# Performance work log

Measured on AMD Instinct MI355X. Metric: run time of the kernel, lower is better.

## Reference

```python
import jax, jax.numpy as jnp
import numpy as np

H = 16  # num_heads

def setup_inputs() -> dict:
    key = jax.random.key(0)
    ks = jax.random.split(key, 9)
    B, S, E = 2, 2048, 1024
    d = E // H  # 64, shared KV head dim
    sc = lambda n: 1.0 / np.sqrt(n)
    return {
        "x": jax.random.normal(ks[0], (B, S, E), jnp.float32),
        "wq": jax.random.normal(ks[1], (E, E), jnp.float32) * sc(E),
        "bq": jax.random.normal(ks[2], (E,), jnp.float32) * 0.02,
        "wk": jax.random.normal(ks[3], (E, d), jnp.float32) * sc(E),
        "bk": jax.random.normal(ks[4], (d,), jnp.float32) * 0.02,
        "wv": jax.random.normal(ks[5], (E, d), jnp.float32) * sc(E),
        "bv": jax.random.normal(ks[6], (d,), jnp.float32) * 0.02,
        "wo": jax.random.normal(ks[7], (E, E), jnp.float32) * sc(E),
        "bo": jax.random.normal(ks[8], (E,), jnp.float32) * 0.02,
    }

def reference(x, wq, bq, wk, bk, wv, bv, wo, bo):
    B, S, E = x.shape
    d = E // H
    Q = (x @ wq + bq).reshape(B, S, H, d).transpose(0, 2, 1, 3)  # [B,H,S,d]
    K = x @ wk + bk  # [B,S,d] shared across heads (MQA)
    V = x @ wv + bv  # [B,S,d]
    scores = jnp.einsum('bhqd,bkd->bhqk', Q, K) / np.sqrt(d)  # [B,H,S,S]
    weights = jax.nn.softmax(scores, axis=-1)
    attn = jnp.einsum('bhqk,bkd->bhqd', weights, V)  # [B,H,S,d]
    # FAITHFUL to source: reshape [B,H,S,d] -> [B,S,E] WITHOUT permuting back
    attn = attn.reshape(B, S, E)
    return attn @ wo + bo
```

## Files before the change

kernel.cpp:

```cpp
#include <hip/hip_runtime.h>
#include <hip/hip_bf16.h>

#define BB 2
#define SS 2048
#define EE 1024
#define HH 16
#define DD 64

using bfrag  = __attribute__((ext_vector_type(8))) short;
using bfrag4 = __attribute__((ext_vector_type(4))) short;
using ffrag  = __attribute__((ext_vector_type(4))) float;
using uint2v = __attribute__((ext_vector_type(2))) uint;

#define MFMA32(A, B, C) __builtin_amdgcn_mfma_f32_16x16x32_bf16(A, B, C, 0, 0, 0)
#define MFMA16(A, B, C) __builtin_amdgcn_mfma_f32_16x16x16bf16_1k(A, B, C, 0, 0, 0)

static __device__ __forceinline__ ushort f2bf(float f) {
  __hip_bfloat16 h = __float2bfloat16(f);
  return *reinterpret_cast<ushort*>(&h);
}

static __device__ __forceinline__ uint pack_bf2(float lo, float hi) {
  uint a = __float_as_uint(lo) + 0x8000u;
  uint b = __float_as_uint(hi) + 0x8000u;
  return __builtin_amdgcn_perm(b, a, 0x07060302u);
}

static __device__ __forceinline__ void gl_lds16(const ushort* g, ushort* l) {
  __builtin_amdgcn_global_load_lds(
      (const __attribute__((address_space(1))) void*)g,
      (__attribute__((address_space(3))) void*)l, 16, 0, 0);
}

__global__ __launch_bounds__(256) void prep(
    const float* __restrict__ x, const float* __restrict__ wq,
    const float* __restrict__ wk, const float* __restrict__ wv,
    const float* __restrict__ wo, ushort* __restrict__ xb,
    ushort* __restrict__ wqkvT, ushort* __restrict__ woT) {
  __shared__ float t[32][33];
  int id = blockIdx.x;
  if (id < 4096) {
    int i = id * 256 + threadIdx.x;
    float4 v = ((const float4*)x)[i];
    ushort4 u = { f2bf(v.x), f2bf(v.y), f2bf(v.z), f2bf(v.w) };
    ((ushort4*)xb)[i] = u;
    return;
  }
  id -= 4096;
  const float* src;
  ushort* dst;
  int N, bx, by;
  if (id < 1024)      { src = wq; dst = wqkvT;                      N = 1024; bx = id & 31;          by = id >> 5; }
  else if (id < 2048) { src = wo; dst = woT;                        N = 1024; bx = (id - 1024) & 31; by = (id - 1024) >> 5; }
  else if (id < 2112) { src = wk; dst = wqkvT + (size_t)1024 * 1024; N = 64;  bx = (id - 2048) & 1;  by = (id - 2048) >> 1; }
  else                { src = wv; dst = wqkvT + (size_t)1088 * 1024; N = 64;  bx = (id - 2112) & 1;  by = (id - 2112) >> 1; }
  const int k0 = by * 32, n0 = bx * 32;
  const int tx = threadIdx.x & 31, ty = threadIdx.x >> 5;
  #pragma unroll
  for (int i = 0; i < 32; i += 8)
    t[ty + i][tx] = src[(size_t)(k0 + ty + i) * N + n0 + tx];
  __syncthreads();
  #pragma unroll
  for (int i = 0; i < 32; i += 8)
    dst[(size_t)(n0 + ty + i) * 1024 + k0 + tx] = f2bf(t[tx][ty + i]);
}

template <bool QKV>
__global__ __launch_bounds__(256) void gemm_mfma3(
    const ushort* __restrict__ A, const ushort* __restrict__ Bt,
    const float* __restrict__ bias0, const float* __restrict__ bias1,
    const float* __restrict__ bias2, void* __restrict__ O1,
    ushort* __restrict__ Kb, ushort* __restrict__ VTb,
    int M, int N, int K, float qscale) {
  __shared__ __align__(16) ushort As[2][128 * 64];
  __shared__ __align__(16) ushort Bs[2][64 * 64];
  const int tid = threadIdx.x;
  const int lane = tid & 63;
  const int quad = lane >> 4;
  const int c = lane & 15;
  const int wv = tid >> 6;
  const int wm = (wv & 1) * 64;
  const int wn = (wv >> 1) * 32;
  const size_t m0 = (size_t)blockIdx.y * 128;
  const size_t n0 = (size_t)blockIdx.x * 64;

  const int srow = lane >> 3;
  const int sck = (lane & 7) ^ srow;

  ffrag zero = {0.f, 0.f, 0.f, 0.f};
  ffrag acc[4][2];
  #pragma unroll
  for (int mt = 0; mt < 4; ++mt)
    #pragma unroll
    for (int nt = 0; nt < 2; ++nt) acc[mt][nt] = zero;

  const int NK = K >> 6;
  #pragma unroll
  for (int i = 0; i < 4; ++i) {
    int ia = wv * 4 + i;
    gl_lds16(&A[(m0 + ia * 8 + srow) * (size_t)K + sck * 8], &As[0][ia * 512]);
  }
  #pragma unroll
  for (int i = 0; i < 2; ++i) {
    int ib = wv * 2 + i;
    gl_lds16(&Bt[(n0 + ib * 8 + srow) * (size_t)K + sck * 8], &Bs[0][ib * 512]);
  }
  __syncthreads();

  for (int ki = 0; ki < NK; ++ki) {
    const int buf = ki & 1;
    if (ki + 1 < NK) {
      int k0 = (ki + 1) << 6;
      #pragma unroll
      for (int i = 0; i < 4; ++i) {
        int ia = wv * 4 + i;
        gl_lds16(&A[(m0 + ia * 8 + srow) * (size_t)K + k0 + sck * 8],
                 &As[buf ^ 1][ia * 512]);
      }
      #pragma unroll
      for (int i = 0; i < 2; ++i) {
        int ib = wv * 2 + i;
        gl_lds16(&Bt[(n0 + ib * 8 + srow) * (size_t)K + k0 + sck * 8],
                 &Bs[buf ^ 1][ib * 512]);
      }
    }
    #pragma unroll
    for (int ks = 0; ks < 2; ++ks) {
      bfrag af[4], bf[2];
      #pragma unroll
      for (int mt = 0; mt < 4; ++mt) {
        int ra = wm + mt * 16 + c;
        af[mt] = *(const bfrag*)&As[buf][(ra * 8 + ((ks * 4 + quad) ^ (ra & 7))) * 8];
      }
      #pragma unroll
      for (int nt = 0; nt < 2; ++nt) {
        int rb = wn + nt * 16 + c;
        bf[nt] = *(const bfrag*)&Bs[buf][(rb * 8 + ((ks * 4 + quad) ^ (rb & 7))) * 8];
      }
      #pragma unroll
      for (int mt = 0; mt < 4; ++mt)
        #pragma unroll
        for (int nt = 0; nt < 2; ++nt)
          acc[mt][nt] = MFMA32(af[mt], bf[nt], acc[mt][nt]);
    }
    __syncthreads();
  }

  #pragma unroll
  for (int nt = 0; nt < 2; ++nt) {
    const int colb = (int)n0 + wn + nt * 16;
    if (QKV) {
      if (colb < 1024) {
        float bb = bias0[colb + c];
        ushort* dst = (ushort*)O1 + colb;
        #pragma unroll
        for (int mt = 0; mt < 4; ++mt)
          #pragma unroll
          for (int r = 0; r < 4; ++r) {
            size_t row = m0 + wm + mt * 16 + quad * 4 + r;
            dst[row * 1024 + c] = f2bf((acc[mt][nt][r] + bb) * qscale);
          }
      } else if (colb < 1088) {
        float bb = bias1[colb - 1024 + c];
        ushort* dst = Kb + (colb - 1024);
        #pragma unroll
        for (int mt = 0; mt < 4; ++mt)
          #pragma unroll
          for (int r = 0; r < 4; ++r) {
            size_t row = m0 + wm + mt * 16 + quad * 4 + r;
            dst[row * 64 + c] = f2bf(acc[mt][nt][r] + bb);
          }
      } else {
        int d = colb - 1088 + c;
        float bb = bias2[colb - 1088 + c];
        int bidx = (int)(m0 >> 11);
        ushort* dstv = VTb + ((size_t)(bidx * 64 + d)) * SS;
        #pragma unroll
        for (int mt = 0; mt < 4; ++mt) {
          int sb = (int)(m0 & 2047) + wm + mt * 16 + quad * 4;
          uint2v u;
          u.x = pack_bf2(acc[mt][nt][0] + bb, acc[mt][nt][1] + bb);
          u.y = pack_bf2(acc[mt][nt][2] + bb, acc[mt][nt][3] + bb);
          *(uint2v*)&dstv[sb] = u;
        }
      }
    } else {
      float bb = bias0[colb + c];
      float* dst = (float*)O1;
      #pragma unroll
      for (int mt = 0; mt < 4; ++mt)
        #pragma unroll
        for (int r = 0; r < 4; ++r) {
          size_t row = m0 + wm + mt * 16 + quad * 4 + r;
          dst[row * (size_t)N + colb + c] = acc[mt][nt][r] + bb;
        }
    }
  }
}

__global__ __launch_bounds__(512) void mqa_attn11(
    const ushort* __restrict__ Q, const ushort* __restrict__ Kg,
    const ushort* __restrict__ VT, ushort* __restrict__ A2) {
  __shared__ __align__(16) ushort Vt[2][2][4096];
  __shared__ float lbuf[512];
  const int tid = threadIdx.x;
  const int lane = tid & 63;
  const int quad = lane >> 4;
  const int c = lane & 15;
  const int wv = tid >> 6;
  const int half = wv >> 2;
  const int lw = wv & 3;
  const int bid = blockIdx.x;
  const int b = bid >> 8;
  const int r = bid & 255;
  const int h = r >> 4;
  const int s0 = (r & 15) << 7;

  const int srow = lane >> 3;
  const int sck = (lane & 7) ^ srow;

  ffrag zero = {0.f, 0.f, 0.f, 0.f};
  bfrag4 ones4;
  #pragma unroll
  for (int i = 0; i < 4; ++i) ones4[i] = (short)16256;

  bfrag aq[2][2];
  #pragma unroll
  for (int mt = 0; mt < 2; ++mt) {
    const ushort* qp =
        Q + ((size_t)(b * SS) + s0 + lw * 32 + mt * 16 + c) * EE + h * 64 + quad * 8;
    aq[mt][0] = *(const bfrag*)qp;
    aq[mt][1] = *(const bfrag*)(qp + 32);
  }

  ffrag o[2][4];
  #pragma unroll
  for (int mt = 0; mt < 2; ++mt)
    #pragma unroll
    for (int nt = 0; nt < 4; ++nt) o[mt][nt] = zero;
  ffrag ls[2] = {zero, zero};

  const int koff = half << 10;
  const ushort* Kbase = Kg + (size_t)b * SS * 64;
  const ushort* Vbase = VT + (size_t)b * 64 * SS;
  const int i0 = lw * 2, i1 = lw * 2 + 1;
  const int r0 = i0 * 8 + srow, r1 = i1 * 8 + srow;

  gl_lds16(Vbase + (size_t)r0 * SS + koff + sck * 8, &Vt[half][0][i0 * 512]);
  gl_lds16(Vbase + (size_t)r1 * SS + koff + sck * 8, &Vt[half][0][i1 * 512]);
  __syncthreads();

  for (int it = 0; it < 16; ++it) {
    const int buf = it & 1;
    if (it + 1 < 16) {
      int kb = koff + ((it + 1) << 6);
      gl_lds16(Vbase + (size_t)r0 * SS + kb + sck * 8, &Vt[half][buf ^ 1][i0 * 512]);
      gl_lds16(Vbase + (size_t)r1 * SS + kb + sck * 8, &Vt[half][buf ^ 1][i1 * 512]);
    }

    #pragma unroll
    for (int kt = 0; kt < 4; ++kt) {
      const int key = koff + (it << 6) + kt * 16 + c;
      const ushort* kp = Kbase + (size_t)key * 64 + quad * 8;
      bfrag kf0 = *(const bfrag*)kp;
      bfrag kf1 = *(const bfrag*)(kp + 32);
      bfrag4 pb[2];
      #pragma unroll
      for (int mt = 0; mt < 2; ++mt) {
        ffrag st = MFMA32(kf0, aq[mt][0], zero);
        st = MFMA32(kf1, aq[mt][1], st);
        uint2v uu;
        uu.x = pack_bf2(__builtin_amdgcn_exp2f(st[0]),
                        __builtin_amdgcn_exp2f(st[1]));
        uu.y = pack_bf2(__builtin_amdgcn_exp2f(st[2]),
                        __builtin_amdgcn_exp2f(st[3]));
        pb[mt] = __builtin_bit_cast(bfrag4, uu);
      }
      const int ck = kt * 2 + (quad >> 1);
      const int wc = (quad & 1) * 4;
      #pragma unroll
      for (int nt = 0; nt < 4; ++nt) {
        int d = nt * 16 + c;
        bfrag4 vf = *(const bfrag4*)&Vt[half][buf][(d * 8 + (ck ^ (d & 7))) * 8 + wc];
        #pragma unroll
        for (int mt = 0; mt < 2; ++mt)
          o[mt][nt] = MFMA16(vf, pb[mt], o[mt][nt]);
      }
      #pragma unroll
      for (int mt = 0; mt < 2; ++mt)
        ls[mt] = MFMA16(ones4, pb[mt], ls[mt]);
    }
    __syncthreads();
  }

  float* cbuf = (float*)&Vt[0][0][0];
  if (half == 1) {
    float* wb = cbuf + (size_t)lw * 2048;
    #pragma unroll
    for (int mt = 0; mt < 2; ++mt) {
      #pragma unroll
      for (int nt = 0; nt < 4; ++nt)
        *(ffrag*)&wb[(mt * 4 + nt) * 256 + lane * 4] = o[mt][nt];
      lbuf[lw * 128 + mt * 64 + lane] = ls[mt][0];
    }
  }
  __syncthreads();
  if (half == 1) return;

  const float* rb = cbuf + (size_t)lw * 2048;
  #pragma unroll
  for (int mt = 0; mt < 2; ++mt) {
    #pragma unroll
    for (int nt = 0; nt < 4; ++nt) {
      ffrag p = *(const ffrag*)&rb[(mt * 4 + nt) * 256 + lane * 4];
      o[mt][nt] += p;
    }
    const float inv = 1.f / (ls[mt][0] + lbuf[lw * 128 + mt * 64 + lane]);
    const int sp = h * 128 + (s0 >> 4) + lw * 2 + mt;
    ushort* orow = A2 + ((size_t)b * SS + sp) * EE;
    #pragma unroll
    for (int nt = 0; nt < 4; ++nt) {
      uint2v u;
      u.x = pack_bf2(o[mt][nt][0] * inv, o[mt][nt][1] * inv);
      u.y = pack_bf2(o[mt][nt][2] * inv, o[mt][nt][3] * inv);
      *(uint2v*)&orow[c * 64 + nt * 16 + quad * 4] = u;
    }
  }
}

extern "C" void kernel_launch(void* const* d_in, const int* in_sizes, int n_in,
                              void* d_out, int out_size, void* d_ws, size_t ws_size,
                              hipStream_t stream) {
  const float* x  = (const float*)d_in[0];
  const float* wq = (const float*)d_in[1];
  const float* bq = (const float*)d_in[2];
  const float* wk = (const float*)d_in[3];
  const float* bk = (const float*)d_in[4];
  const float* wv = (const float*)d_in[5];
  const float* bv = (const float*)d_in[6];
  const float* wo = (const float*)d_in[7];
  const float* bo = (const float*)d_in[8];
  float* out = (float*)d_out;

  char* w = (char*)d_ws;
  ushort* xb     = (ushort*)w;  w += (size_t)4096 * 1024 * 2;
  ushort* wqkvT  = (ushort*)w;  w += (size_t)1152 * 1024 * 2;
  ushort* woT    = (ushort*)w;  w += (size_t)1024 * 1024 * 2;
  ushort* Qb     = (ushort*)w;  w += (size_t)4096 * 1024 * 2;
  ushort* Kb     = (ushort*)w;  w += (size_t)4096 * 64 * 2;
  ushort* VTb    = (ushort*)w;  w += (size_t)BB * 64 * SS * 2;
  ushort* A2     = (ushort*)w;  w += (size_t)4096 * 1024 * 2;

  prep<<<6272, 256, 0, stream>>>(x, wq, wk, wv, wo, xb, wqkvT, woT);

  const float qscale = 0.18033688011112042f;
  gemm_mfma3<true><<<dim3(18, 32), 256, 0, stream>>>(
      xb, wqkvT, bq, bk, bv, Qb, Kb, VTb, 4096, 1152, 1024, qscale);

  mqa_attn11<<<512, 512, 0, stream>>>(Qb, Kb, VTb, A2);

  gemm_mfma3<false><<<dim3(16, 32), 256, 0, stream>>>(
      A2, woT, bo, nullptr, nullptr, out, nullptr, nullptr, 4096, 1024, 1024, 1.0f);
}
```

Baseline: 199.0 us.

## Stage K tiles in LDS and remap GEMM blocks across XCDs

```diff
diff --git a/kernel.cpp b/kernel.cpp
--- a/kernel.cpp
+++ b/kernel.cpp
@@ -11,6 +11,7 @@
 using bfrag4 = __attribute__((ext_vector_type(4))) short;
 using ffrag  = __attribute__((ext_vector_type(4))) float;
 using uint2v = __attribute__((ext_vector_type(2))) uint;
+using uint4v = __attribute__((ext_vector_type(4))) uint;
 
 #define MFMA32(A, B, C) __builtin_amdgcn_mfma_f32_16x16x32_bf16(A, B, C, 0, 0, 0)
 #define MFMA16(A, B, C) __builtin_amdgcn_mfma_f32_16x16x16bf16_1k(A, B, C, 0, 0, 0)
@@ -81,8 +82,15 @@
   const int wv = tid >> 6;
   const int wm = (wv & 1) * 64;
   const int wn = (wv >> 1) * 32;
-  const size_t m0 = (size_t)blockIdx.y * 128;
-  const size_t n0 = (size_t)blockIdx.x * 64;
+
+  const int gx = gridDim.x, gy = gridDim.y;
+  const int lid = blockIdx.y * gx + blockIdx.x;
+  const int xcd = lid & 7;
+  const int idx = lid >> 3;
+  const int mrow = xcd * (gy >> 3) + idx / gx;
+  const int ncol = idx % gx;
+  const size_t m0 = (size_t)mrow * 128;
+  const size_t n0 = (size_t)ncol * 64;
 
   const int srow = lane >> 3;
   const int sck = (lane & 7) ^ srow;
@@ -198,10 +206,10 @@
   }
 }
 
-__global__ __launch_bounds__(512) void mqa_attn11(
+__global__ __launch_bounds__(512, 8) void mqa_attn13(
     const ushort* __restrict__ Q, const ushort* __restrict__ Kg,
     const ushort* __restrict__ VT, ushort* __restrict__ A2) {
-  __shared__ __align__(16) ushort Vt[2][2][4096];
+  __shared__ __align__(16) ushort KV[2][2][4096];
   __shared__ float lbuf[512];
   const int tid = threadIdx.x;
   const int lane = tid & 63;
@@ -243,27 +251,40 @@
   const int koff = half << 10;
   const ushort* Kbase = Kg + (size_t)b * SS * 64;
   const ushort* Vbase = VT + (size_t)b * 64 * SS;
-  const int i0 = lw * 2, i1 = lw * 2 + 1;
-  const int r0 = i0 * 8 + srow, r1 = i1 * 8 + srow;
-
-  gl_lds16(Vbase + (size_t)r0 * SS + koff + sck * 8, &Vt[half][0][i0 * 512]);
-  gl_lds16(Vbase + (size_t)r1 * SS + koff + sck * 8, &Vt[half][0][i1 * 512]);
+  const int kr = lw * 8 + srow;
+
+  const int jj = lane & 3;
+  const int d0 = lw * 16 + (lane >> 2);
+  const ushort* vsrc = Vbase + (size_t)d0 * SS + jj * 8;
+  const int q00 = d0 * 32 + (((jj * 2)     ^ (d0 & 7)) * 4);
+  const int q01 = d0 * 32 + (((jj * 2 + 1) ^ (d0 & 7)) * 4);
+
+  {
+    uint4v v0 = *(const uint4v*)(vsrc + koff);
+    gl_lds16(Kbase + (size_t)(koff + kr) * 64 + sck * 8, &KV[half][0][lw * 512]);
+    ushort* vdst = &KV[half][0][2048];
+    *(uint2v*)&vdst[q00] = (uint2v){v0[0], v0[1]};
+    *(uint2v*)&vdst[q01] = (uint2v){v0[2], v0[3]};
+  }
   __syncthreads();
 
-  for (int it = 0; it < 16; ++it) {
+  for (int it = 0; it < 32; ++it) {
     const int buf = it & 1;
-    if (it + 1 < 16) {
-      int kb = koff + ((it + 1) << 6);
-      gl_lds16(Vbase + (size_t)r0 * SS + kb + sck * 8, &Vt[half][buf ^ 1][i0 * 512]);
-      gl_lds16(Vbase + (size_t)r1 * SS + kb + sck * 8, &Vt[half][buf ^ 1][i1 * 512]);
-    }
-
-    #pragma unroll
-    for (int kt = 0; kt < 4; ++kt) {
-      const int key = koff + (it << 6) + kt * 16 + c;
-      const ushort* kp = Kbase + (size_t)key * 64 + quad * 8;
-      bfrag kf0 = *(const bfrag*)kp;
-      bfrag kf1 = *(const bfrag*)(kp + 32);
+    uint4v nv;
+    if (it + 1 < 32) {
+      int kb = koff + ((it + 1) << 5);
+      nv = *(const uint4v*)(vsrc + kb);
+      gl_lds16(Kbase + (size_t)(kb + kr) * 64 + sck * 8, &KV[half][buf ^ 1][lw * 512]);
+    }
+    const ushort* Kt = &KV[half][buf][0];
+    const ushort* Vt = &KV[half][buf][2048];
+
+    #pragma unroll
+    for (int kt = 0; kt < 2; ++kt) {
+      const int key = kt * 16 + c;
+      const int k7 = key & 7;
+      bfrag kf0 = *(const bfrag*)&Kt[(key * 8 + (quad ^ k7)) * 8];
+      bfrag kf1 = *(const bfrag*)&Kt[(key * 8 + ((quad + 4) ^ k7)) * 8];
       bfrag4 pb[2];
       #pragma unroll
       for (int mt = 0; mt < 2; ++mt) {
@@ -276,12 +297,11 @@
                         __builtin_amdgcn_exp2f(st[3]));
         pb[mt] = __builtin_bit_cast(bfrag4, uu);
       }
-      const int ck = kt * 2 + (quad >> 1);
-      const int wc = (quad & 1) * 4;
+      const int vg = kt * 4 + quad;
       #pragma unroll
       for (int nt = 0; nt < 4; ++nt) {
         int d = nt * 16 + c;
-        bfrag4 vf = *(const bfrag4*)&Vt[half][buf][(d * 8 + (ck ^ (d & 7))) * 8 + wc];
+        bfrag4 vf = *(const bfrag4*)&Vt[d * 32 + ((vg ^ (d & 7)) * 4)];
         #pragma unroll
         for (int mt = 0; mt < 2; ++mt)
           o[mt][nt] = MFMA16(vf, pb[mt], o[mt][nt]);
@@ -290,10 +310,16 @@
       for (int mt = 0; mt < 2; ++mt)
         ls[mt] = MFMA16(ones4, pb[mt], ls[mt]);
     }
+
+    if (it + 1 < 32) {
+      ushort* vdst = &KV[half][buf ^ 1][2048];
+      *(uint2v*)&vdst[q00] = (uint2v){nv[0], nv[1]};
+      *(uint2v*)&vdst[q01] = (uint2v){nv[2], nv[3]};
+    }
     __syncthreads();
   }
 
-  float* cbuf = (float*)&Vt[0][0][0];
+  float* cbuf = (float*)&KV[0][0][0];
   if (half == 1) {
     float* wb = cbuf + (size_t)lw * 2048;
     #pragma unroll
@@ -357,7 +383,7 @@
   gemm_mfma3<true><<<dim3(18, 32), 256, 0, stream>>>(
       xb, wqkvT, bq, bk, bv, Qb, Kb, VTb, 4096, 1152, 1024, qscale);
 
-  mqa_attn11<<<512, 512, 0, stream>>>(Qb, Kb, VTb, A2);
+  mqa_attn13<<<512, 512, 0, stream>>>(Qb, Kb, VTb, A2);
 
   gemm_mfma3<false><<<dim3(16, 32), 256, 0, stream>>>(
       A2, woT, bo, nullptr, nullptr, out, nullptr, nullptr, 4096, 1024, 1024, 1.0f);
```

Result: slower. 500.5 us (+151.5%).
